# Performance work log

Measured on AMD Instinct MI355X. Metric: run time of the kernel, lower is better.

The kernel has to match this reference:

```python
import jax, jax.numpy as jnp
import numpy as np

Q = 1024   # number of HMM states
A = 26     # alphabet size
B = 128    # batch
L = 1024   # sequence length


def setup_inputs() -> dict:
    key = jax.random.key(0)
    k1, k2, k3, k4 = jax.random.split(key, 4)
    inputs = jax.random.uniform(k1, (B, L, A), dtype=jnp.float32)  # soft one-hot observations
    init_logits = jax.random.normal(k2, (Q,), dtype=jnp.float32)
    trans_logits = jax.random.normal(k3, (Q, Q), dtype=jnp.float32)
    emis_logits = jax.random.normal(k4, (Q, A), dtype=jnp.float32)
    return {"inputs": inputs, "init_logits": init_logits,
            "trans_logits": trans_logits, "emis_logits": emis_logits}


def reference(inputs, init_logits, trans_logits, emis_logits):
    # Build valid HMM parameters (cell.init_cell materializes probability kernels)
    pi = jax.nn.softmax(init_logits)                 # [Q] initial state distribution
    T = jax.nn.softmax(trans_logits, axis=-1)        # [Q,Q] transition matrix (rows sum to 1)
    Bm = jax.nn.softmax(emis_logits, axis=-1)        # [Q,A] emission matrix

    # Per-step emission likelihoods e_t[b,q] = sum_a B[q,a] * inputs[b,t,a]
    E = jnp.einsum('bla,qa->blq', inputs, Bm)        # [B,L,Q]

    # Scaled forward algorithm: alpha normalized each step, loglik accumulates log-scale
    a0 = pi[None, :] * E[:, 0]                       # [B,Q]
    s0 = jnp.sum(a0, axis=-1, keepdims=True)         # [B,1]
    carry0 = (a0 / s0, jnp.log(s0[:, 0]))

    def step(carry, e_t):
        alpha, ll = carry
        a = (alpha @ T) * e_t                        # [B,Q]
        s = jnp.sum(a, axis=-1, keepdims=True)
        return (a / s, ll + jnp.log(s[:, 0])), None

    E_t = jnp.swapaxes(E, 0, 1)                      # [L,B,Q] time-major for scan
    (alpha, loglik), _ = jax.lax.scan(step, carry0, E_t[1:])
    return loglik                                    # [B] log-likelihood per sequence
```

## Files before the change

### kernel.cpp

```cpp
#include <hip/hip_runtime.h>
#include <hip/hip_bf16.h>

#define QD 1024
#define AD 26
#define BD 128
#define LD 1024
#define NWG 128
#define PSTR (8 * 32 * 64 * 8)

typedef short bf16x8 __attribute__((ext_vector_type(8)));
typedef float f32x4 __attribute__((ext_vector_type(4)));

static __device__ __forceinline__ unsigned short f2bf(float f) {
    __hip_bfloat16 h = __float2bfloat16(f);
    return *reinterpret_cast<unsigned short*>(&h);
}

static __device__ __forceinline__ bf16x8 load_a16(const unsigned short* p) {
    unsigned long long lo = __hip_atomic_load((const unsigned long long*)p,
                                              __ATOMIC_RELAXED, __HIP_MEMORY_SCOPE_AGENT);
    unsigned long long hi = __hip_atomic_load((const unsigned long long*)(p + 4),
                                              __ATOMIC_RELAXED, __HIP_MEMORY_SCOPE_AGENT);
    union { unsigned long long q[2]; bf16x8 v; } u;
    u.q[0] = lo; u.q[1] = hi;
    return u.v;
}

static __device__ __forceinline__ void store_a8(unsigned short* p, ushort4 v) {
    union { ushort4 s; unsigned long long q; } u; u.s = v;
    __hip_atomic_store((unsigned long long*)p, u.q,
                       __ATOMIC_RELAXED, __HIP_MEMORY_SCOPE_AGENT);
}

static __device__ __forceinline__ bf16x8 lds_load16(const unsigned short* p) {
    unsigned long long lo = __hip_atomic_load((const unsigned long long*)p,
                                              __ATOMIC_RELAXED, __HIP_MEMORY_SCOPE_WORKGROUP);
    unsigned long long hi = __hip_atomic_load((const unsigned long long*)(p + 4),
                                              __ATOMIC_RELAXED, __HIP_MEMORY_SCOPE_WORKGROUP);
    union { unsigned long long q[2]; bf16x8 v; } u;
    u.q[0] = lo; u.q[1] = hi;
    return u.v;
}
static __device__ __forceinline__ void lds_store16(unsigned short* p, bf16x8 v) {
    union { bf16x8 v; unsigned long long q[2]; } u; u.v = v;
    __hip_atomic_store((unsigned long long*)p, u.q[0],
                       __ATOMIC_RELAXED, __HIP_MEMORY_SCOPE_WORKGROUP);
    __hip_atomic_store((unsigned long long*)(p + 4), u.q[1],
                       __ATOMIC_RELAXED, __HIP_MEMORY_SCOPE_WORKGROUP);
}

__global__ void softmax_pack_T(const float* __restrict__ tl, unsigned short* __restrict__ tf) {
    const int i = blockIdx.x;
    const int tid = threadIdx.x;
    __shared__ float red[256];
    float v[4];
    float m = -1e30f;
    for (int c = 0; c < 4; ++c) { v[c] = tl[i * QD + tid + 256 * c]; m = fmaxf(m, v[c]); }
    red[tid] = m; __syncthreads();
    for (int s = 128; s > 0; s >>= 1) { if (tid < s) red[tid] = fmaxf(red[tid], red[tid + s]); __syncthreads(); }
    m = red[0]; __syncthreads();
    float sum = 0.f;
    for (int c = 0; c < 4; ++c) { v[c] = expf(v[c] - m); sum += v[c]; }
    red[tid] = sum; __syncthreads();
    for (int s = 128; s > 0; s >>= 1) { if (tid < s) red[tid] += red[tid + s]; __syncthreads(); }
    const float inv = 1.0f / red[0];
    const int kt = i >> 5, quad = (i >> 3) & 3, j = i & 7;
    for (int c = 0; c < 4; ++c) {
        const int q = tid + 256 * c;
        const int mt = q >> 4, col = q & 15;
        tf[(size_t)((mt * 32 + kt) * 64 + quad * 16 + col) * 8 + j] = f2bf(v[c] * inv);
    }
}

__global__ void softmax_pack_B(const float* __restrict__ el, unsigned short* __restrict__ bmf) {
    const int q = blockIdx.x * blockDim.x + threadIdx.x;
    if (q >= QD) return;
    float v[AD];
    float m = -1e30f;
    for (int a = 0; a < AD; ++a) { v[a] = el[q * AD + a]; m = fmaxf(m, v[a]); }
    float sum = 0.f;
    for (int a = 0; a < AD; ++a) { v[a] = expf(v[a] - m); sum += v[a]; }
    const float inv = 1.0f / sum;
    const int mt = q >> 4, col = q & 15;
    for (int a = 0; a < 32; ++a) {
        const float val = (a < AD) ? v[a] * inv : 0.f;
        bmf[(size_t)(mt * 64 + (a >> 3) * 16 + col) * 8 + (a & 7)] = f2bf(val);
    }
}

__global__ void softmax_pi(const float* __restrict__ il, float* __restrict__ pi) {
    const int tid = threadIdx.x;
    __shared__ float red[1024];
    const float v = il[tid];
    red[tid] = v; __syncthreads();
    for (int s = 512; s > 0; s >>= 1) { if (tid < s) red[tid] = fmaxf(red[tid], red[tid + s]); __syncthreads(); }
    const float m = red[0]; __syncthreads();
    const float e = expf(v - m);
    red[tid] = e; __syncthreads();
    for (int s = 512; s > 0; s >>= 1) { if (tid < s) red[tid] += red[tid + s]; __syncthreads(); }
    pi[tid] = e / red[0];
}

__launch_bounds__(256, 1)
__global__ void hmm_scan(const float* __restrict__ inputs,
                         const unsigned short* __restrict__ tf,
                         const unsigned short* __restrict__ bmf,
                         const float* __restrict__ pi,
                         unsigned short* __restrict__ apack,
                         float* __restrict__ out) {
    const int tid   = threadIdx.x;
    const int mtl   = tid >> 6;
    const int lane  = tid & 63;
    const int quad  = lane >> 4;
    const int col   = lane & 15;
    const int qs    = (int)blockIdx.x >> 3;
    const int grp   = (int)blockIdx.x & 7;
    const int b     = (grp >> 1) * 32 + (grp & 1) * 16 + col;
    const int qrow  = qs * 64 + mtl * 16 + quad * 4;

    __shared__ unsigned short lbuf[2][32][512];
    {
        unsigned int* lp = (unsigned int*)lbuf;
        #pragma unroll
        for (int i = 0; i < 64; ++i) lp[tid + 256 * i] = 0xAAAAAAAAu;
        __syncthreads();
    }

    const int lane_c = ((mtl & 1) * 2 + (quad >> 1)) * 16 + col;
    const size_t poff = (size_t)((grp * 32 + qs * 2 + (mtl >> 1)) * 64 + lane_c) * 8 + (quad & 1) * 4;
    const size_t coff = (size_t)(grp * 32) * 512 + (size_t)lane * 8;

    bf16x8 tfr[32];
    {
        const bf16x8* tsrc = (const bf16x8*)tf + (size_t)(qs * 4 + mtl) * 32 * 64 + lane;
        #pragma unroll
        for (int kt = 0; kt < 32; ++kt) tfr[kt] = tsrc[(size_t)kt * 64];
    }
    const bf16x8 bmA = *(const bf16x8*)&bmf[(size_t)((qs * 4 + mtl) * 64 + lane) * 8];
    float pr[4];
    #pragma unroll
    for (int r = 0; r < 4; ++r) pr[r] = pi[qrow + r];

    bf16x8 ones;
    #pragma unroll
    for (int i = 0; i < 8; ++i) ones[i] = (short)0x3F80;

    const f32x4 fz = {0.f, 0.f, 0.f, 0.f};
    const unsigned M = 0x80008000u;
    float ll = 0.f;

    f32x4 e;
    {
        bf16x8 xb;
        #pragma unroll
        for (int j = 0; j < 8; ++j) {
            const int a = quad * 8 + j;
            const float v = (a < AD) ? inputs[(size_t)b * LD * AD + a] : 0.f;
            xb[j] = (short)f2bf(v);
        }
        e = __builtin_amdgcn_mfma_f32_16x16x32_bf16(bmA, xb, fz, 0, 0, 0);
    }

    f32x4 acc = fz, on = fz;

    for (int t = 0; t < LD; ++t) {
        float v0[4];
        if (t == 0) {
            #pragma unroll
            for (int r = 0; r < 4; ++r) v0[r] = pr[r] * e[r];
        } else {
            const float i0 = 1.f / on[0];
            #pragma unroll
            for (int r = 0; r < 4; ++r) v0[r] = acc[r] * e[r] * i0;
        }
        const unsigned short tagbit = (unsigned short)(((t >> 1) & 1) << 15);
        ushort4 s0;
        s0.x = f2bf(v0[0]); s0.y = f2bf(v0[1]);
        s0.z = (unsigned short)(f2bf(v0[2]) | tagbit);
        s0.w = (unsigned short)(f2bf(v0[3]) | tagbit);
        store_a8(apack + (size_t)(t & 1) * PSTR + poff, s0);

        if (qs == 0 && mtl == 0 && t > 0) ll += logf(on[0]);

        if (t + 1 < LD) {
            bf16x8 xb;
            #pragma unroll
            for (int j = 0; j < 8; ++j) {
                const int a = quad * 8 + j;
                const float v = (a < AD)
                    ? inputs[((size_t)b * LD + (t + 1)) * AD + a] : 0.f;
                xb[j] = (short)f2bf(v);
            }
            e = __builtin_amdgcn_mfma_f32_16x16x32_bf16(bmA, xb, fz, 0, 0, 0);

            const unsigned short* cp = apack + (size_t)(t & 1) * PSTR + coff;
            const unsigned E = ((t >> 1) & 1) ? M : 0u;

            bf16x8 bufr[8];
            unsigned bad;
            do {
                #pragma unroll
                for (int k = 0; k < 8; ++k)
                    bufr[k] = load_a16(cp + (size_t)(mtl * 8 + k) * 512);
                bad = 0u;
                #pragma unroll
                for (int k = 0; k < 8; ++k) {
                    union { bf16x8 v; uint4 u; } w; w.v = bufr[k];
                    bad |= (w.u.x | w.u.z | (w.u.y ^ E) | (w.u.w ^ E)) & M;
                }
            } while (__ballot(bad == 0u) != ~0ULL);

            #pragma unroll
            for (int k = 0; k < 8; ++k)
                lds_store16(&lbuf[t & 1][mtl * 8 + k][lane * 8], bufr[k]);

            acc = fz; on = fz;
            #pragma unroll
            for (int g = 0; g < 4; ++g) {
                if (g == mtl) {
                    #pragma unroll
                    for (int k = 0; k < 8; ++k) {
                        union { bf16x8 v; uint4 u; } w; w.v = bufr[k];
                        w.u.x &= ~M; w.u.y &= ~M; w.u.z &= ~M; w.u.w &= ~M;
                        acc = __builtin_amdgcn_mfma_f32_16x16x32_bf16(tfr[g * 8 + k], w.v, acc, 0, 0, 0);
                        on  = __builtin_amdgcn_mfma_f32_16x16x32_bf16(ones, w.v, on, 0, 0, 0);
                    }
                } else {
                    bf16x8 lb[8];
                    do {
                        #pragma unroll
                        for (int k = 0; k < 8; ++k)
                            lb[k] = lds_load16(&lbuf[t & 1][g * 8 + k][lane * 8]);
                        bad = 0u;
                        #pragma unroll
                        for (int k = 0; k < 8; ++k) {
                            union { bf16x8 v; uint4 u; } w; w.v = lb[k];
                            bad |= (w.u.x | w.u.z | (w.u.y ^ E) | (w.u.w ^ E)) & M;
                        }
                    } while (__ballot(bad == 0u) != ~0ULL);
                    #pragma unroll
                    for (int k = 0; k < 8; ++k) {
                        union { bf16x8 v; uint4 u; } w; w.v = lb[k];
                        w.u.x &= ~M; w.u.y &= ~M; w.u.z &= ~M; w.u.w &= ~M;
                        acc = __builtin_amdgcn_mfma_f32_16x16x32_bf16(tfr[g * 8 + k], w.v, acc, 0, 0, 0);
                        on  = __builtin_amdgcn_mfma_f32_16x16x32_bf16(ones, w.v, on, 0, 0, 0);
                    }
                }
            }
        }
    }

    if (qs == 0 && mtl == 0) {
        const unsigned short* cp = apack + (size_t)((LD - 1) & 1) * PSTR + coff;
        const unsigned E = (((LD - 1) >> 1) & 1) ? M : 0u;
        f32x4 f0 = fz;
        #pragma unroll
        for (int h = 0; h < 2; ++h) {
            bf16x8 bufr[16];
            unsigned bad;
            do {
                #pragma unroll
                for (int k = 0; k < 16; ++k)
                    bufr[k] = load_a16(cp + (size_t)(h * 16 + k) * 512);
                bad = 0u;
                #pragma unroll
                for (int k = 0; k < 16; ++k) {
                    union { bf16x8 v; uint4 u; } w; w.v = bufr[k];
                    bad |= (w.u.x | w.u.z | (w.u.y ^ E) | (w.u.w ^ E)) & M;
                }
            } while (__ballot(bad == 0u) != ~0ULL);
            #pragma unroll
            for (int k = 0; k < 16; ++k) {
                union { bf16x8 v; uint4 u; } w; w.v = bufr[k];
                w.u.x &= ~M; w.u.y &= ~M; w.u.z &= ~M; w.u.w &= ~M;
                f0 = __builtin_amdgcn_mfma_f32_16x16x32_bf16(ones, w.v, f0, 0, 0, 0);
            }
        }
        if (quad == 0) out[b] = ll + logf(f0[0]);
    }
}

extern "C" void kernel_launch(void* const* d_in, const int* in_sizes, int n_in,
                              void* d_out, int out_size, void* d_ws, size_t ws_size,
                              hipStream_t stream) {
    const float* inputs       = (const float*)d_in[0];
    const float* init_logits  = (const float*)d_in[1];
    const float* trans_logits = (const float*)d_in[2];
    const float* emis_logits  = (const float*)d_in[3];
    float* out = (float*)d_out;

    unsigned short* tf    = (unsigned short*)d_ws;
    unsigned short* bmf   = tf + (size_t)QD * QD;
    float* pi             = (float*)(bmf + (size_t)QD * 32);
    unsigned short* apack = (unsigned short*)(pi + QD);

    hipMemsetAsync(apack, 0xAA, (size_t)2 * PSTR * sizeof(unsigned short), stream);

    softmax_pack_T<<<1024, 256, 0, stream>>>(trans_logits, tf);
    softmax_pack_B<<<4, 256, 0, stream>>>(emis_logits, bmf);
    softmax_pi<<<1, 1024, 0, stream>>>(init_logits, pi);

    hmm_scan<<<NWG, 256, 0, stream>>>(inputs, tf, bmf, pi, apack, out);
}
```

Before: 2.909 ms.

## Per-chunk polling with early LDS forwarding, split accumulators, and fast reciprocal

The global poll loop now tracks which of its eight 16-byte chunks are already valid. Only stale chunks are reloaded, and each valid chunk is written to LDS at once, so the other waves no longer wait for all eight. The LDS buffer is split into separate lo/hi 64-bit arrays. The MFMA chains are split into two interleaved accumulators to shorten the dependency chain. The 1/x uses the hardware rcp. The gain is lower per-step synchronisation latency in exchange for more complex control flow and divergent branches inside the spin loop.

New measurement: 3.679 ms. 26.5% more time.

```diff
diff --git a/kernel.cpp b/kernel.cpp
--- a/kernel.cpp
+++ b/kernel.cpp
@@ -30,23 +30,6 @@
     union { ushort4 s; unsigned long long q; } u; u.s = v;
     __hip_atomic_store((unsigned long long*)p, u.q,
                        __ATOMIC_RELAXED, __HIP_MEMORY_SCOPE_AGENT);
-}
-
-static __device__ __forceinline__ bf16x8 lds_load16(const unsigned short* p) {
-    unsigned long long lo = __hip_atomic_load((const unsigned long long*)p,
-                                              __ATOMIC_RELAXED, __HIP_MEMORY_SCOPE_WORKGROUP);
-    unsigned long long hi = __hip_atomic_load((const unsigned long long*)(p + 4),
-                                              __ATOMIC_RELAXED, __HIP_MEMORY_SCOPE_WORKGROUP);
-    union { unsigned long long q[2]; bf16x8 v; } u;
-    u.q[0] = lo; u.q[1] = hi;
-    return u.v;
-}
-static __device__ __forceinline__ void lds_store16(unsigned short* p, bf16x8 v) {
-    union { bf16x8 v; unsigned long long q[2]; } u; u.v = v;
-    __hip_atomic_store((unsigned long long*)p, u.q[0],
-                       __ATOMIC_RELAXED, __HIP_MEMORY_SCOPE_WORKGROUP);
-    __hip_atomic_store((unsigned long long*)(p + 4), u.q[1],
-                       __ATOMIC_RELAXED, __HIP_MEMORY_SCOPE_WORKGROUP);
 }
 
 __global__ void softmax_pack_T(const float* __restrict__ tl, unsigned short* __restrict__ tf) {
@@ -118,11 +101,16 @@
     const int b     = (grp >> 1) * 32 + (grp & 1) * 16 + col;
     const int qrow  = qs * 64 + mtl * 16 + quad * 4;
 
-    __shared__ unsigned short lbuf[2][32][512];
+    __shared__ unsigned long long llo[2][32][64];
+    __shared__ unsigned long long lhi[2][32][64];
     {
-        unsigned int* lp = (unsigned int*)lbuf;
+        unsigned long long* p0 = &llo[0][0][0];
+        unsigned long long* p1 = &lhi[0][0][0];
         #pragma unroll
-        for (int i = 0; i < 64; ++i) lp[tid + 256 * i] = 0xAAAAAAAAu;
+        for (int i = 0; i < 16; ++i) {
+            p0[tid + 256 * i] = 0xAAAAAAAAAAAAAAAAULL;
+            p1[tid + 256 * i] = 0xAAAAAAAAAAAAAAAAULL;
+        }
         __syncthreads();
     }
 
@@ -146,7 +134,7 @@
     for (int i = 0; i < 8; ++i) ones[i] = (short)0x3F80;
 
     const f32x4 fz = {0.f, 0.f, 0.f, 0.f};
-    const unsigned M = 0x80008000u;
+    const unsigned long long MQ = 0x8000800080008000ULL;
     float ll = 0.f;
 
     f32x4 e;
@@ -161,17 +149,19 @@
         e = __builtin_amdgcn_mfma_f32_16x16x32_bf16(bmA, xb, fz, 0, 0, 0);
     }
 
-    f32x4 acc = fz, on = fz;
+    f32x4 accA = fz, accB = fz, onA = fz, onB = fz;
 
     for (int t = 0; t < LD; ++t) {
         float v0[4];
+        float on0 = 0.f;
         if (t == 0) {
             #pragma unroll
             for (int r = 0; r < 4; ++r) v0[r] = pr[r] * e[r];
         } else {
-            const float i0 = 1.f / on[0];
-            #pragma unroll
-            for (int r = 0; r < 4; ++r) v0[r] = acc[r] * e[r] * i0;
+            on0 = onA[0] + onB[0];
+            const float i0 = __builtin_amdgcn_rcpf(on0);
+            #pragma unroll
+            for (int r = 0; r < 4; ++r) v0[r] = (accA[r] + accB[r]) * e[r] * i0;
         }
         const unsigned short tagbit = (unsigned short)(((t >> 1) & 1) << 15);
         ushort4 s0;
@@ -180,7 +170,7 @@
         s0.w = (unsigned short)(f2bf(v0[3]) | tagbit);
         store_a8(apack + (size_t)(t & 1) * PSTR + poff, s0);
 
-        if (qs == 0 && mtl == 0 && t > 0) ll += logf(on[0]);
+        if (qs == 0 && mtl == 0 && t > 0) ll += logf(on0);
 
         if (t + 1 < LD) {
             bf16x8 xb;
@@ -193,57 +183,84 @@
             }
             e = __builtin_amdgcn_mfma_f32_16x16x32_bf16(bmA, xb, fz, 0, 0, 0);
 
-            const unsigned short* cp = apack + (size_t)(t & 1) * PSTR + coff;
-            const unsigned E = ((t >> 1) & 1) ? M : 0u;
+            const int p = t & 1;
+            const unsigned short* cp = apack + (size_t)p * PSTR + coff;
+            const unsigned E32 = ((t >> 1) & 1) ? 0x80008000u : 0u;
+            const unsigned long long EQ = ((unsigned long long)E32) << 32;
 
             bf16x8 bufr[8];
-            unsigned bad;
+            unsigned vmask = 0u;
             do {
-                #pragma unroll
-                for (int k = 0; k < 8; ++k)
-                    bufr[k] = load_a16(cp + (size_t)(mtl * 8 + k) * 512);
-                bad = 0u;
+                unsigned long long tlo[8], thi[8];
                 #pragma unroll
                 for (int k = 0; k < 8; ++k) {
-                    union { bf16x8 v; uint4 u; } w; w.v = bufr[k];
-                    bad |= (w.u.x | w.u.z | (w.u.y ^ E) | (w.u.w ^ E)) & M;
+                    if (!(vmask & (1u << k))) {
+                        const unsigned long long* gp =
+                            (const unsigned long long*)(cp + (size_t)(mtl * 8 + k) * 512);
+                        tlo[k] = __hip_atomic_load(gp,     __ATOMIC_RELAXED, __HIP_MEMORY_SCOPE_AGENT);
+                        thi[k] = __hip_atomic_load(gp + 1, __ATOMIC_RELAXED, __HIP_MEMORY_SCOPE_AGENT);
+                    }
                 }
-            } while (__ballot(bad == 0u) != ~0ULL);
-
-            #pragma unroll
-            for (int k = 0; k < 8; ++k)
-                lds_store16(&lbuf[t & 1][mtl * 8 + k][lane * 8], bufr[k]);
-
-            acc = fz; on = fz;
+                #pragma unroll
+                for (int k = 0; k < 8; ++k) {
+                    if (!(vmask & (1u << k))) {
+                        const unsigned long long bad =
+                            (((tlo[k] ^ EQ) | (thi[k] ^ EQ)) & MQ);
+                        if (bad == 0ULL) {
+                            __hip_atomic_store(&llo[p][mtl * 8 + k][lane], tlo[k],
+                                               __ATOMIC_RELAXED, __HIP_MEMORY_SCOPE_WORKGROUP);
+                            __hip_atomic_store(&lhi[p][mtl * 8 + k][lane], thi[k],
+                                               __ATOMIC_RELAXED, __HIP_MEMORY_SCOPE_WORKGROUP);
+                            union { unsigned long long q[2]; bf16x8 v; } u;
+                            u.q[0] = tlo[k] & ~MQ; u.q[1] = thi[k] & ~MQ;
+                            bufr[k] = u.v;
+                            vmask |= 1u << k;
+                        }
+                    }
+                }
+            } while (__ballot(vmask == 0xffu) != ~0ULL);
+
+            accA = fz; accB = fz; onA = fz; onB = fz;
             #pragma unroll
             for (int g = 0; g < 4; ++g) {
                 if (g == mtl) {
                     #pragma unroll
                     for (int k = 0; k < 8; ++k) {
-                        union { bf16x8 v; uint4 u; } w; w.v = bufr[k];
-                        w.u.x &= ~M; w.u.y &= ~M; w.u.z &= ~M; w.u.w &= ~M;
-                        acc = __builtin_amdgcn_mfma_f32_16x16x32_bf16(tfr[g * 8 + k], w.v, acc, 0, 0, 0);
-                        on  = __builtin_amdgcn_mfma_f32_16x16x32_bf16(ones, w.v, on, 0, 0, 0);
+                        if (k & 1) {
+                            accB = __builtin_amdgcn_mfma_f32_16x16x32_bf16(tfr[g * 8 + k], bufr[k], accB, 0, 0, 0);
+                            onB  = __builtin_amdgcn_mfma_f32_16x16x32_bf16(ones, bufr[k], onB, 0, 0, 0);
+                        } else {
+                            accA = __builtin_amdgcn_mfma_f32_16x16x32_bf16(tfr[g * 8 + k], bufr[k], accA, 0, 0, 0);
+                            onA  = __builtin_amdgcn_mfma_f32_16x16x32_bf16(ones, bufr[k], onA, 0, 0, 0);
+                        }
                     }
                 } else {
-                    bf16x8 lb[8];
+                    unsigned long long slo[8], shi[8];
+                    unsigned long long badq;
                     do {
                         #pragma unroll
+                        for (int k = 0; k < 8; ++k) {
+                            slo[k] = __hip_atomic_load(&llo[p][g * 8 + k][lane],
+                                                       __ATOMIC_RELAXED, __HIP_MEMORY_SCOPE_WORKGROUP);
+                            shi[k] = __hip_atomic_load(&lhi[p][g * 8 + k][lane],
+                                                       __ATOMIC_RELAXED, __HIP_MEMORY_SCOPE_WORKGROUP);
+                        }
+                        badq = 0ULL;
+                        #pragma unroll
                         for (int k = 0; k < 8; ++k)
-                            lb[k] = lds_load16(&lbuf[t & 1][g * 8 + k][lane * 8]);
-                        bad = 0u;
-                        #pragma unroll
-                        for (int k = 0; k < 8; ++k) {
-                            union { bf16x8 v; uint4 u; } w; w.v = lb[k];
-                            bad |= (w.u.x | w.u.z | (w.u.y ^ E) | (w.u.w ^ E)) & M;
-                        }
-                    } while (__ballot(bad == 0u) != ~0ULL);
+                            badq |= (((slo[k] ^ EQ) | (shi[k] ^ EQ)) & MQ);
+                    } while (__ballot(badq == 0ULL) != ~0ULL);
                     #pragma unroll
                     for (int k = 0; k < 8; ++k) {
-                        union { bf16x8 v; uint4 u; } w; w.v = lb[k];
-                        w.u.x &= ~M; w.u.y &= ~M; w.u.z &= ~M; w.u.w &= ~M;
-                        acc = __builtin_amdgcn_mfma_f32_16x16x32_bf16(tfr[g * 8 + k], w.v, acc, 0, 0, 0);
-                        on  = __builtin_amdgcn_mfma_f32_16x16x32_bf16(ones, w.v, on, 0, 0, 0);
+                        union { unsigned long long q[2]; bf16x8 v; } u;
+                        u.q[0] = slo[k] & ~MQ; u.q[1] = shi[k] & ~MQ;
+                        if (k & 1) {
+                            accB = __builtin_amdgcn_mfma_f32_16x16x32_bf16(tfr[g * 8 + k], u.v, accB, 0, 0, 0);
+                            onB  = __builtin_amdgcn_mfma_f32_16x16x32_bf16(ones, u.v, onB, 0, 0, 0);
+                        } else {
+                            accA = __builtin_amdgcn_mfma_f32_16x16x32_bf16(tfr[g * 8 + k], u.v, accA, 0, 0, 0);
+                            onA  = __builtin_amdgcn_mfma_f32_16x16x32_bf16(ones, u.v, onA, 0, 0, 0);
+                        }
                     }
                 }
             }
@@ -252,27 +269,28 @@
 
     if (qs == 0 && mtl == 0) {
         const unsigned short* cp = apack + (size_t)((LD - 1) & 1) * PSTR + coff;
-        const unsigned E = (((LD - 1) >> 1) & 1) ? M : 0u;
+        const unsigned E32 = (((LD - 1) >> 1) & 1) ? 0x80008000u : 0u;
+        const unsigned long long EQ = ((unsigned long long)E32) << 32;
         f32x4 f0 = fz;
         #pragma unroll
         for (int h = 0; h < 2; ++h) {
             bf16x8 bufr[16];
-            unsigned bad;
+            unsigned long long badq;
             do {
                 #pragma unroll
                 for (int k = 0; k < 16; ++k)
                     bufr[k] = load_a16(cp + (size_t)(h * 16 + k) * 512);
-                bad = 0u;
+                badq = 0ULL;
                 #pragma unroll
                 for (int k = 0; k < 16; ++k) {
-                    union { bf16x8 v; uint4 u; } w; w.v = bufr[k];
-                    bad |= (w.u.x | w.u.z | (w.u.y ^ E) | (w.u.w ^ E)) & M;
+                    union { bf16x8 v; unsigned long long q[2]; } w; w.v = bufr[k];
+                    badq |= (((w.q[0] ^ EQ) | (w.q[1] ^ EQ)) & MQ);
                 }
-            } while (__ballot(bad == 0u) != ~0ULL);
+            } while (__ballot(badq == 0ULL) != ~0ULL);
             #pragma unroll
             for (int k = 0; k < 16; ++k) {
-                union { bf16x8 v; uint4 u; } w; w.v = bufr[k];
-                w.u.x &= ~M; w.u.y &= ~M; w.u.z &= ~M; w.u.w &= ~M;
+                union { bf16x8 v; unsigned long long q[2]; } w; w.v = bufr[k];
+                w.q[0] &= ~MQ; w.q[1] &= ~MQ;
                 f0 = __builtin_amdgcn_mfma_f32_16x16x32_bf16(ones, w.v, f0, 0, 0, 0);
             }
         }
```
